# Optimization experiments

Hardware: AMD Instinct MI355X
Metric: run time of the kernel (lower is better)

Reference implementation:

```python
import jax, jax.numpy as jnp
import numpy as np

B, G, IN, OUT, H, W = 8, 3, 384, 384, 64, 64
CG, OG = IN // G, OUT // G  # channels per group


def setup_inputs() -> dict:
    key = jax.random.key(0)
    ks = jax.random.split(key, 6)
    return {
        "input": jax.random.normal(ks[0], (B, IN, H, W), jnp.float32),
        "wh_pred": jax.random.uniform(ks[1], (B, 2 * G, H, W), jnp.float32),
        # conv_offset: 1x1 grouped conv, groups=G, in=2 per group, out=18 per group
        "w_off": jax.random.normal(ks[2], (G, 18, 2), jnp.float32) * 0.1,
        "b_off": jax.random.normal(ks[3], (G, 18), jnp.float32) * 0.1,
        # deformable 3x3 conv, groups=G: weight [OUT, IN/G, 3, 3]
        "w_d": jax.random.normal(ks[4], (OUT, CG, 3, 3), jnp.float32) * (1.0 / np.sqrt(CG * 9)),
        "b_d": jax.random.normal(ks[5], (OUT,), jnp.float32) * 0.01,
    }


def _bilinear_sample(img, py, px):
    # img: [Cg, H, W]; py, px: [9, H, W] float sampling positions
    # zero padding outside bounds (torchvision deform_conv2d semantics)
    y0 = jnp.floor(py)
    x0 = jnp.floor(px)
    wy = py - y0  # weight toward y0+1
    wx = px - x0
    y0i = y0.astype(jnp.int32)
    x0i = x0.astype(jnp.int32)

    def gather(yi, xi):
        valid = (yi >= 0) & (yi < H) & (xi >= 0) & (xi < W)
        yc = jnp.clip(yi, 0, H - 1)
        xc = jnp.clip(xi, 0, W - 1)
        v = img[:, yc, xc]  # [Cg, 9, H, W]
        return v * valid[None].astype(img.dtype)

    v00 = gather(y0i, x0i)
    v01 = gather(y0i, x0i + 1)
    v10 = gather(y0i + 1, x0i)
    v11 = gather(y0i + 1, x0i + 1)
    return (v00 * ((1 - wy) * (1 - wx))[None]
            + v01 * ((1 - wy) * wx)[None]
            + v10 * (wy * (1 - wx))[None]
            + v11 * (wy * wx)[None])  # [Cg, 9, H, W]


def _forward(input, wh_pred, w_off, b_off, w_d, b_d):
    # conv_offset: grouped 1x1 conv on detached wh_pred
    wh = jax.lax.stop_gradient(wh_pred).reshape(B, G, 2, H, W)
    off = jnp.einsum('bgchw,goc->bgohw', wh, w_off) + b_off[None, :, :, None, None]
    off = off.reshape(B, G, 9, 2, H, W)  # (dy, dx) per kernel tap

    # sampling positions for 3x3 kernel, stride 1, pad 1
    ky = (jnp.arange(9) // 3 - 1).astype(jnp.float32)
    kx = (jnp.arange(9) % 3 - 1).astype(jnp.float32)
    hh = jnp.arange(H, dtype=jnp.float32)
    ww = jnp.arange(W, dtype=jnp.float32)
    py = off[:, :, :, 0] + hh[None, None, None, :, None] + ky[None, None, :, None, None]
    px = off[:, :, :, 1] + ww[None, None, None, None, :] + kx[None, None, :, None, None]

    xg = input.reshape(B, G, CG, H, W)
    samp = jax.vmap(jax.vmap(_bilinear_sample))(xg, py, px)  # [B, G, Cg, 9, H, W]

    wg = w_d.reshape(G, OG, CG, 9)
    out = jnp.einsum('bgckhw,gock->bgohw', samp, wg)
    out = out.reshape(B, OUT, H, W) + b_d[None, :, None, None]
    return out


def reference(input, wh_pred, w_off, b_off, w_d, b_d):
    return _forward(input, wh_pred, w_off, b_off, w_d, b_d)
```

## Files before the change

kernel.cpp:

```cpp
#include <hip/hip_runtime.h>


typedef __attribute__((ext_vector_type(8))) short short8;
typedef __attribute__((ext_vector_type(4))) float floatx4;
typedef __attribute__((ext_vector_type(4))) unsigned int uintx4;

#define SLAB 524288
#define XT_GUARD 8704
#define XT_TAIL 512

__device__ __forceinline__ float bf_lo(unsigned int d) {
  return __uint_as_float(d << 16);
}
__device__ __forceinline__ float bf_hi(unsigned int d) {
  return __uint_as_float(d & 0xffff0000u);
}
__device__ __forceinline__ unsigned int cvtpk_bf16(float lo, float hi) {
  unsigned int r;
  asm("v_cvt_pk_bf16_f32 %0, %1, %2" : "=v"(r) : "v"(lo), "v"(hi));
  return r;
}

__global__ __launch_bounds__(256) void transpose_x_kernel(
    const float* __restrict__ in, ushort* __restrict__ xT) {
  __shared__ float tile[32][33];
  const int t  = threadIdx.x;
  const int tx = t & 31, ty = t >> 5;
  const int bx = blockIdx.x;
  const int x0 = (bx & 1) * 32;
  const int c0 = (bx >> 1) * 32;
  const int y  = blockIdx.y;
  const int bg = blockIdx.z;
  const int b  = bg / 3, g = bg % 3;

  const float* src = in + ((size_t)(b * 384 + g * 128)) * 4096 + (size_t)y * 64;
#pragma unroll
  for (int it = 0; it < 4; ++it) {
    int c = c0 + ty + it * 8;
    tile[ty + it * 8][tx] = src[(size_t)c * 4096 + x0 + tx];
  }
  __syncthreads();
  ushort* dst = xT + (((size_t)bg * 64 + y) * 64) * 128;
#pragma unroll
  for (int it = 0; it < 4; ++it) {
    int x = x0 + ty + it * 8;
    float v = tile[tx][ty + it * 8];
    dst[(size_t)x * 128 + c0 + tx] =
        (ushort)((__float_as_uint(v) + 0x8000u) >> 16);
  }
}

__global__ __launch_bounds__(256) void swizzle_w_kernel(
    const float* __restrict__ w_d, ushort* __restrict__ wB) {
  int idx = blockIdx.x * 256 + threadIdx.x;
  if (idx >= 442368) return;
  int j  = idx & 7;
  int l  = (idx >> 3) & 63;
  int f  = (idx >> 9) & 7;
  int s  = (idx >> 12) & 3;
  int t2 = idx >> 14;
  int k  = t2 % 9;
  int g  = t2 / 9;
  int o  = f * 16 + (l & 15);
  int c  = s * 32 + (l >> 4) * 8 + j;
  float v = w_d[((size_t)(g * 128 + o) * 128 + c) * 9 + k];
  wB[idx] = (ushort)((__float_as_uint(v) + 0x8000u) >> 16);
}

__global__ __launch_bounds__(256) void fa_main_mfma(
    const ushort* __restrict__ xT, const ushort* __restrict__ wB,
    const float* __restrict__ wh_pred, const float* __restrict__ w_off,
    const float* __restrict__ b_off, const float* __restrict__ b_d,
    float* __restrict__ out) {
  __shared__ int    off_s[9][32];
  __shared__ float4 w4_s[9][32];
  __shared__ ushort samp[2][32][128];

  const int t   = threadIdx.x;
  const int bid = blockIdx.x;
  const int b   = bid & 7;
  const int rem = bid >> 3;
  const int ph  = rem & 1;
  const int h   = (rem >> 1) & 63;
  const int g   = rem >> 7;
  const int pos0 = ph * 32;

  for (int idx = t; idx < 288; idx += 256) {
    int k = idx >> 5, pos = idx & 31;
    int posg = pos0 + pos;
    float wh0 = wh_pred[(((size_t)b * 6 + g * 2 + 0) * 64 + h) * 64 + posg];
    float wh1 = wh_pred[(((size_t)b * 6 + g * 2 + 1) * 64 + h) * 64 + posg];
    int oy_i = g * 18 + k * 2;
    int ox_i = oy_i + 1;
    float oy = fmaf(w_off[oy_i * 2], wh0, fmaf(w_off[oy_i * 2 + 1], wh1, b_off[oy_i]));
    float ox = fmaf(w_off[ox_i * 2], wh0, fmaf(w_off[ox_i * 2 + 1], wh1, b_off[ox_i]));
    float py = oy + (float)(h + k / 3 - 1);
    float px = ox + (float)(posg + k % 3 - 1);

    float fy = floorf(py), fx = floorf(px);
    int y0 = (int)fy, x0 = (int)fx;
    float wy = py - fy, wx = px - fx;
    float m_y0 = ((unsigned)y0 < 64u) ? 1.f : 0.f;
    float m_y1 = ((unsigned)(y0 + 1) < 64u) ? 1.f : 0.f;
    float m_x0 = ((unsigned)x0 < 64u) ? 1.f : 0.f;
    float m_x1 = ((unsigned)(x0 + 1) < 64u) ? 1.f : 0.f;
    float4 w4;
    w4.x = (1.f - wy) * (1.f - wx) * m_y0 * m_x0;
    w4.y = (1.f - wy) * wx * m_y0 * m_x1;
    w4.z = wy * (1.f - wx) * m_y1 * m_x0;
    w4.w = wy * wx * m_y1 * m_x1;
    int y0c = min(max(y0, -1), 63);
    int x0c = min(max(x0, -1), 63);
    off_s[k][pos] = (y0c * 64 + x0c) * 128;
    w4_s[k][pos]  = w4;
  }
  __syncthreads();

  const int wv  = t >> 6;
  const int l   = t & 63;
  const int l15 = l & 15;
  const int lhi = l >> 4;

  floatx4 acc[2][2];
#pragma unroll
  for (int ia = 0; ia < 2; ++ia) {
#pragma unroll
    for (int r = 0; r < 4; ++r) {
      float bias = b_d[g * 128 + wv * 32 + ia * 16 + lhi * 4 + r];
#pragma unroll
      for (int jb = 0; jb < 2; ++jb) acc[ia][jb][r] = bias;
    }
  }

  const int spos16 = t >> 4;
  const int lane16 = t & 15;
  const ushort* xb = xT + (size_t)(b * 3 + g) * SLAB;
  const ushort* wg = wB + (size_t)g * 9 * 16384;

  auto stage = [&](int k, ushort(*sb)[128]) {
#pragma unroll
    for (int p = 0; p < 2; ++p) {
      int pos = p * 16 + spos16;
      int off = off_s[k][pos];
      float4 w4 = w4_s[k][pos];
      const ushort* p00 = xb + off + lane16 * 8;
      uintx4 a00 = *(const uintx4*)(p00);
      uintx4 a01 = *(const uintx4*)(p00 + 128);
      uintx4 a10 = *(const uintx4*)(p00 + 8192);
      uintx4 a11 = *(const uintx4*)(p00 + 8320);
      uintx4 pk;
#pragma unroll
      for (int d = 0; d < 4; ++d) {
        float lo = fmaf(bf_lo(a11[d]), w4.w, fmaf(bf_lo(a10[d]), w4.z,
                   fmaf(bf_lo(a01[d]), w4.y, bf_lo(a00[d]) * w4.x)));
        float hi = fmaf(bf_hi(a11[d]), w4.w, fmaf(bf_hi(a10[d]), w4.z,
                   fmaf(bf_hi(a01[d]), w4.y, bf_hi(a00[d]) * w4.x)));
        pk[d] = cvtpk_bf16(lo, hi);
      }
      *(uintx4*)&sb[pos][(lane16 * 8) ^ ((pos & 7) << 3)] = pk;
    }
  };

  auto mfma_phase = [&](int k, const ushort(*sb)[128]) {
    const ushort* wk = wg + (size_t)k * 16384;
#pragma unroll
    for (int s = 0; s < 4; ++s) {
      short8 a0 = *(const short8*)(wk + ((s * 8 + wv * 2 + 0) * 64 + l) * 8);
      short8 a1 = *(const short8*)(wk + ((s * 8 + wv * 2 + 1) * 64 + l) * 8);
      const int cb = (s * 32 + lhi * 8) ^ ((l15 & 7) << 3);
#pragma unroll
      for (int jb = 0; jb < 2; ++jb) {
        short8 bf = *(const short8*)&sb[jb * 16 + l15][cb];
        acc[0][jb] = __builtin_amdgcn_mfma_f32_16x16x32_bf16(a0, bf, acc[0][jb], 0, 0, 0);
        acc[1][jb] = __builtin_amdgcn_mfma_f32_16x16x32_bf16(a1, bf, acc[1][jb], 0, 0, 0);
      }
    }
  };

  stage(0, samp[0]);
  __syncthreads();
  for (int k = 0; k < 9; ++k) {
    if (k < 8) stage(k + 1, samp[(k + 1) & 1]);
    mfma_phase(k, samp[k & 1]);
    __syncthreads();
  }

#pragma unroll
  for (int ia = 0; ia < 2; ++ia) {
#pragma unroll
    for (int jb = 0; jb < 2; ++jb) {
#pragma unroll
      for (int r = 0; r < 4; ++r) {
        int o = wv * 32 + ia * 16 + lhi * 4 + r;
        int pos = pos0 + jb * 16 + l15;
        out[(((size_t)(b * 384 + g * 128 + o)) * 64 + h) * 64 + pos] = acc[ia][jb][r];
      }
    }
  }
}

extern "C" void kernel_launch(void* const* d_in, const int* in_sizes, int n_in,
                              void* d_out, int out_size, void* d_ws, size_t ws_size,
                              hipStream_t stream) {
  const float* input   = (const float*)d_in[0];
  const float* wh_pred = (const float*)d_in[1];
  const float* w_off   = (const float*)d_in[2];
  const float* b_off   = (const float*)d_in[3];
  const float* w_d     = (const float*)d_in[4];
  const float* b_d     = (const float*)d_in[5];
  float* out = (float*)d_out;

  ushort* xT = (ushort*)d_ws + XT_GUARD;
  ushort* wB = xT + (size_t)24 * SLAB + XT_TAIL;

  transpose_x_kernel<<<dim3(8, 64, 24), 256, 0, stream>>>(input, xT);
  swizzle_w_kernel<<<dim3(1728), 256, 0, stream>>>(w_d, wB);
  fa_main_mfma<<<dim3(3072), 256, 0, stream>>>(
      xT, wB, wh_pred, w_off, b_off, b_d, out);
}
```

Baseline: 89.81 us.

## Process full 64-pixel rows per 512-thread block with fp16 bilinear weights

Each block now covers a whole output row of 64 positions with 8 waves, each wave owning 16 output channels, where before each block covered half a row with 4 waves. Per-block weight loads are now amortized over twice as many pixels, and the offset/weight setup is done once per row instead of twice. Bilinear weights are stored in LDS as fp16 to cut LDS footprint, and s_setprio is raised around the MFMA phase to favor matrix issue. This costs fewer, larger blocks, more LDS per block, and slight precision loss in the interpolation weights.

```diff
diff --git a/kernel.cpp b/kernel.cpp
--- a/kernel.cpp
+++ b/kernel.cpp
@@ -19,6 +19,13 @@
   unsigned int r;
   asm("v_cvt_pk_bf16_f32 %0, %1, %2" : "=v"(r) : "v"(lo), "v"(hi));
   return r;
+}
+__device__ __forceinline__ ushort f2h(float x) {
+  _Float16 h = (_Float16)x;
+  return __builtin_bit_cast(ushort, h);
+}
+__device__ __forceinline__ float h2f(ushort u) {
+  return (float)__builtin_bit_cast(_Float16, u);
 }
 
 __global__ __launch_bounds__(256) void transpose_x_kernel(
@@ -67,35 +74,32 @@
   wB[idx] = (ushort)((__float_as_uint(v) + 0x8000u) >> 16);
 }
 
-__global__ __launch_bounds__(256) void fa_main_mfma(
+__global__ __launch_bounds__(512) void fa_main_mfma(
     const ushort* __restrict__ xT, const ushort* __restrict__ wB,
     const float* __restrict__ wh_pred, const float* __restrict__ w_off,
     const float* __restrict__ b_off, const float* __restrict__ b_d,
     float* __restrict__ out) {
-  __shared__ int    off_s[9][32];
-  __shared__ float4 w4_s[9][32];
-  __shared__ ushort samp[2][32][128];
+  __shared__ int     off_s[9][64];
+  __shared__ ushort4 w4h_s[9][64];
+  __shared__ ushort  samp[2][64][128];
 
   const int t   = threadIdx.x;
   const int bid = blockIdx.x;
   const int b   = bid & 7;
   const int rem = bid >> 3;
-  const int ph  = rem & 1;
-  const int h   = (rem >> 1) & 63;
-  const int g   = rem >> 7;
-  const int pos0 = ph * 32;
-
-  for (int idx = t; idx < 288; idx += 256) {
-    int k = idx >> 5, pos = idx & 31;
-    int posg = pos0 + pos;
-    float wh0 = wh_pred[(((size_t)b * 6 + g * 2 + 0) * 64 + h) * 64 + posg];
-    float wh1 = wh_pred[(((size_t)b * 6 + g * 2 + 1) * 64 + h) * 64 + posg];
+  const int g   = rem >> 6;
+  const int h   = rem & 63;
+
+  for (int idx = t; idx < 576; idx += 512) {
+    int k = idx >> 6, pos = idx & 63;
+    float wh0 = wh_pred[(((size_t)b * 6 + g * 2 + 0) * 64 + h) * 64 + pos];
+    float wh1 = wh_pred[(((size_t)b * 6 + g * 2 + 1) * 64 + h) * 64 + pos];
     int oy_i = g * 18 + k * 2;
     int ox_i = oy_i + 1;
     float oy = fmaf(w_off[oy_i * 2], wh0, fmaf(w_off[oy_i * 2 + 1], wh1, b_off[oy_i]));
     float ox = fmaf(w_off[ox_i * 2], wh0, fmaf(w_off[ox_i * 2 + 1], wh1, b_off[ox_i]));
     float py = oy + (float)(h + k / 3 - 1);
-    float px = ox + (float)(posg + k % 3 - 1);
+    float px = ox + (float)(pos + k % 3 - 1);
 
     float fy = floorf(py), fx = floorf(px);
     int y0 = (int)fy, x0 = (int)fx;
@@ -104,15 +108,15 @@
     float m_y1 = ((unsigned)(y0 + 1) < 64u) ? 1.f : 0.f;
     float m_x0 = ((unsigned)x0 < 64u) ? 1.f : 0.f;
     float m_x1 = ((unsigned)(x0 + 1) < 64u) ? 1.f : 0.f;
-    float4 w4;
-    w4.x = (1.f - wy) * (1.f - wx) * m_y0 * m_x0;
-    w4.y = (1.f - wy) * wx * m_y0 * m_x1;
-    w4.z = wy * (1.f - wx) * m_y1 * m_x0;
-    w4.w = wy * wx * m_y1 * m_x1;
+    ushort4 w4;
+    w4.x = f2h((1.f - wy) * (1.f - wx) * m_y0 * m_x0);
+    w4.y = f2h((1.f - wy) * wx * m_y0 * m_x1);
+    w4.z = f2h(wy * (1.f - wx) * m_y1 * m_x0);
+    w4.w = f2h(wy * wx * m_y1 * m_x1);
     int y0c = min(max(y0, -1), 63);
     int x0c = min(max(x0, -1), 63);
     off_s[k][pos] = (y0c * 64 + x0c) * 128;
-    w4_s[k][pos]  = w4;
+    w4h_s[k][pos] = w4;
   }
   __syncthreads();
 
@@ -121,18 +125,15 @@
   const int l15 = l & 15;
   const int lhi = l >> 4;
 
-  floatx4 acc[2][2];
-#pragma unroll
-  for (int ia = 0; ia < 2; ++ia) {
-#pragma unroll
-    for (int r = 0; r < 4; ++r) {
-      float bias = b_d[g * 128 + wv * 32 + ia * 16 + lhi * 4 + r];
-#pragma unroll
-      for (int jb = 0; jb < 2; ++jb) acc[ia][jb][r] = bias;
-    }
-  }
-
-  const int spos16 = t >> 4;
+  floatx4 acc[4];
+#pragma unroll
+  for (int r = 0; r < 4; ++r) {
+    float bias = b_d[g * 128 + wv * 16 + lhi * 4 + r];
+#pragma unroll
+    for (int jb = 0; jb < 4; ++jb) acc[jb][r] = bias;
+  }
+
+  const int g16    = t >> 4;
   const int lane16 = t & 15;
   const ushort* xb = xT + (size_t)(b * 3 + g) * SLAB;
   const ushort* wg = wB + (size_t)g * 9 * 16384;
@@ -140,9 +141,10 @@
   auto stage = [&](int k, ushort(*sb)[128]) {
 #pragma unroll
     for (int p = 0; p < 2; ++p) {
-      int pos = p * 16 + spos16;
+      int pos = p * 32 + g16;
       int off = off_s[k][pos];
-      float4 w4 = w4_s[k][pos];
+      ushort4 wq = w4h_s[k][pos];
+      float w00 = h2f(wq.x), w01 = h2f(wq.y), w10 = h2f(wq.z), w11 = h2f(wq.w);
       const ushort* p00 = xb + off + lane16 * 8;
       uintx4 a00 = *(const uintx4*)(p00);
       uintx4 a01 = *(const uintx4*)(p00 + 128);
@@ -151,10 +153,10 @@
       uintx4 pk;
 #pragma unroll
       for (int d = 0; d < 4; ++d) {
-        float lo = fmaf(bf_lo(a11[d]), w4.w, fmaf(bf_lo(a10[d]), w4.z,
-                   fmaf(bf_lo(a01[d]), w4.y, bf_lo(a00[d]) * w4.x)));
-        float hi = fmaf(bf_hi(a11[d]), w4.w, fmaf(bf_hi(a10[d]), w4.z,
-                   fmaf(bf_hi(a01[d]), w4.y, bf_hi(a00[d]) * w4.x)));
+        float lo = fmaf(bf_lo(a11[d]), w11, fmaf(bf_lo(a10[d]), w10,
+                   fmaf(bf_lo(a01[d]), w01, bf_lo(a00[d]) * w00)));
+        float hi = fmaf(bf_hi(a11[d]), w11, fmaf(bf_hi(a10[d]), w10,
+                   fmaf(bf_hi(a01[d]), w01, bf_hi(a00[d]) * w00)));
         pk[d] = cvtpk_bf16(lo, hi);
       }
       *(uintx4*)&sb[pos][(lane16 * 8) ^ ((pos & 7) << 3)] = pk;
@@ -163,18 +165,18 @@
 
   auto mfma_phase = [&](int k, const ushort(*sb)[128]) {
     const ushort* wk = wg + (size_t)k * 16384;
+    __builtin_amdgcn_s_setprio(1);
 #pragma unroll
     for (int s = 0; s < 4; ++s) {
-      short8 a0 = *(const short8*)(wk + ((s * 8 + wv * 2 + 0) * 64 + l) * 8);
-      short8 a1 = *(const short8*)(wk + ((s * 8 + wv * 2 + 1) * 64 + l) * 8);
+      short8 a = *(const short8*)(wk + ((s * 8 + wv) * 64 + l) * 8);
       const int cb = (s * 32 + lhi * 8) ^ ((l15 & 7) << 3);
 #pragma unroll
-      for (int jb = 0; jb < 2; ++jb) {
+      for (int jb = 0; jb < 4; ++jb) {
         short8 bf = *(const short8*)&sb[jb * 16 + l15][cb];
-        acc[0][jb] = __builtin_amdgcn_mfma_f32_16x16x32_bf16(a0, bf, acc[0][jb], 0, 0, 0);
-        acc[1][jb] = __builtin_amdgcn_mfma_f32_16x16x32_bf16(a1, bf, acc[1][jb], 0, 0, 0);
+        acc[jb] = __builtin_amdgcn_mfma_f32_16x16x32_bf16(a, bf, acc[jb], 0, 0, 0);
       }
     }
+    __builtin_amdgcn_s_setprio(0);
   };
 
   stage(0, samp[0]);
@@ -186,15 +188,12 @@
   }
 
 #pragma unroll
-  for (int ia = 0; ia < 2; ++ia) {
-#pragma unroll
-    for (int jb = 0; jb < 2; ++jb) {
-#pragma unroll
-      for (int r = 0; r < 4; ++r) {
-        int o = wv * 32 + ia * 16 + lhi * 4 + r;
-        int pos = pos0 + jb * 16 + l15;
-        out[(((size_t)(b * 384 + g * 128 + o)) * 64 + h) * 64 + pos] = acc[ia][jb][r];
-      }
+  for (int jb = 0; jb < 4; ++jb) {
+#pragma unroll
+    for (int r = 0; r < 4; ++r) {
+      int o = wv * 16 + lhi * 4 + r;
+      int pos = jb * 16 + l15;
+      out[(((size_t)(b * 384 + g * 128 + o)) * 64 + h) * 64 + pos] = acc[jb][r];
     }
   }
 }
@@ -215,6 +214,6 @@
 
   transpose_x_kernel<<<dim3(8, 64, 24), 256, 0, stream>>>(input, xT);
   swizzle_w_kernel<<<dim3(1728), 256, 0, stream>>>(w_d, wB);
-  fa_main_mfma<<<dim3(3072), 256, 0, stream>>>(
+  fa_main_mfma<<<dim3(1536), 512, 0, stream>>>(
       xT, wB, wh_pred, w_off, b_off, b_d, out);
 }
```

Result: faster. 87.32 us (-2.8%).
